# Optimization experiments

Measured on AMD Instinct MI355X. Metric: run time of the kernel, lower is better.

Reference implementation:

```python
import jax, jax.numpy as jnp
import numpy as np

D_MODEL = 1024
N_HEAD = 16
DFF = 4096
N_EXPERTS = 4
DFF_E = DFF // N_EXPERTS  # 1024, per-expert hidden
LN_EPS = 1e-5


def _layer_norm(x, g, b):
    m = jnp.mean(x, axis=-1, keepdims=True)
    v = jnp.mean(jnp.square(x - m), axis=-1, keepdims=True)
    return (x - m) * jax.lax.rsqrt(v + LN_EPS) * g + b


def setup_inputs() -> dict:
    key = jax.random.key(0)
    ks = jax.random.split(key, 16)
    B, S, D = 8, 1024, D_MODEL
    s = 0.02
    return {
        "src": jax.random.normal(ks[0], (B, S, D), jnp.float32),
        "pos_embed": jax.random.normal(ks[1], (B, S, D), jnp.float32),
        # nn.MultiheadAttention packed in-projection [3D, D] and out-projection [D, D]
        "in_proj_w": jax.random.normal(ks[2], (3 * D, D), jnp.float32) * s,
        "in_proj_b": jax.random.normal(ks[3], (3 * D,), jnp.float32) * s,
        "out_proj_w": jax.random.normal(ks[4], (D, D), jnp.float32) * s,
        "out_proj_b": jax.random.normal(ks[5], (D,), jnp.float32) * s,
        # MoE gate Linear(D, E)
        "gate_w": jax.random.normal(ks[6], (N_EXPERTS, D), jnp.float32) * s,
        "gate_b": jax.random.normal(ks[7], (N_EXPERTS,), jnp.float32) * s,
        # per-expert FFN: Linear(D, DFF_E) then Linear(DFF_E, D), stacked over experts
        "w1": jax.random.normal(ks[8], (N_EXPERTS, DFF_E, D), jnp.float32) * s,
        "b1": jax.random.normal(ks[9], (N_EXPERTS, DFF_E), jnp.float32) * s,
        "w2": jax.random.normal(ks[10], (N_EXPERTS, D, DFF_E), jnp.float32) * s,
        "b2": jax.random.normal(ks[11], (N_EXPERTS, D), jnp.float32) * s,
        # LayerNorms
        "ln1_g": jnp.ones((D,), jnp.float32),
        "ln1_b": jnp.zeros((D,), jnp.float32),
        "ln2_g": jnp.ones((D,), jnp.float32),
        "ln2_b": jnp.zeros((D,), jnp.float32),
    }


def reference(src, pos_embed, in_proj_w, in_proj_b, out_proj_w, out_proj_b,
              gate_w, gate_b, w1, b1, w2, b2, ln1_g, ln1_b, ln2_g, ln2_b):
    B, S, D = src.shape
    H, hd = N_HEAD, D // N_HEAD
    residual = src
    # --- self-attention (post-norm path, dropout in eval mode => identity) ---
    qk = src + pos_embed  # q = k = src + pos_embed, value = src
    wq, wk, wv = jnp.split(in_proj_w, 3, axis=0)
    bq, bk, bv = jnp.split(in_proj_b, 3)
    q = (qk @ wq.T + bq).reshape(B, S, H, hd).transpose(0, 2, 1, 3)
    k = (qk @ wk.T + bk).reshape(B, S, H, hd).transpose(0, 2, 1, 3)
    v = (src @ wv.T + bv).reshape(B, S, H, hd).transpose(0, 2, 1, 3)
    scores = jnp.einsum('bhqd,bhkd->bhqk', q, k) / jnp.sqrt(jnp.asarray(hd, q.dtype))
    attn = jax.nn.softmax(scores, axis=-1)
    o = jnp.einsum('bhqk,bhkd->bhqd', attn, v).transpose(0, 2, 1, 3).reshape(B, S, D)
    o = o @ out_proj_w.T + out_proj_b
    x = _layer_norm(residual + o, ln1_g, ln1_b)
    # --- MoE FFN: sample one expert per token from gate softmax ---
    gate_logits = x @ gate_w.T + gate_b  # [B, S, E]
    chosen = jax.random.categorical(jax.random.key(42), gate_logits, axis=-1)  # [B, S] int
    oh = jax.nn.one_hot(chosen, N_EXPERTS, dtype=x.dtype)  # [B, S, E]
    # dense all-expert compute + one-hot select (equals gather/scatter math)
    h = jax.nn.relu(jnp.einsum('bsd,efd->bsef', x, w1) + b1)  # [B,S,E,DFF_E]
    y = jnp.einsum('bsef,edf->bsed', h, w2) + b2              # [B,S,E,D]
    moe_out = jnp.einsum('bsed,bse->bsd', y, oh)
    out = _layer_norm(x + moe_out, ln2_g, ln2_b)
    return out
```

## Files before the change

kernel.cpp:

```cpp
#include <hip/hip_runtime.h>
#include <cstdint>
#include <cstddef>


typedef _Float16 h16;
typedef h16 h16x8 __attribute__((ext_vector_type(8)));
typedef h16 h16x4 __attribute__((ext_vector_type(4)));
typedef __fp16 fp16x2 __attribute__((ext_vector_type(2)));
typedef float f32x4 __attribute__((ext_vector_type(4)));
typedef uint32_t u32;

#define DM 1024
#define NH 16
#define HD 64
#define SEQ 1024
#define BB 8
#define BS (BB*SEQ)
#define NBH (BB*NH)
#define NE 4
#define DFE 1024
#define QB 128
#define NCHUNK 16
#define SLDA 32
#define FLD 72
#define NPOS 9216

#define MFMA16(a,b,c) __builtin_amdgcn_mfma_f32_16x16x32_f16(a,b,c,0,0,0)

static constexpr size_t E = (size_t)BS*DM*2;
static constexpr size_t OFF_QKH = 0;
static constexpr size_t OFF_QKL = E;
static constexpr size_t OFF_SRCH= 2*E;
static constexpr size_t OFF_SRCL= 3*E;
static constexpr size_t OFF_W3H = 4*E;
static constexpr size_t OFF_W3L = 4*E + (size_t)3*DM*DM*2;
static constexpr size_t OFF_WOH = 4*E + (size_t)6*DM*DM*2;
static constexpr size_t OFF_WOL = 4*E + (size_t)7*DM*DM*2;
static constexpr size_t OFF_QH  = 5*E;
static constexpr size_t OFF_QL  = 6*E;
static constexpr size_t OFF_KH  = 7*E;
static constexpr size_t OFF_KL  = 8*E;
static constexpr size_t OFF_VH  = 9*E;
static constexpr size_t OFF_VL  = 10*E;
static constexpr size_t OFF_OH  = 0;
static constexpr size_t OFF_OL  = E;
static constexpr size_t OFF_ATT = 2*E;
static constexpr size_t OFF_X   = 5*E;
static constexpr size_t OFF_XH  = 7*E;
static constexpr size_t OFF_W1H = 8*E;
static constexpr size_t OFF_W2H = 8*E + (size_t)NE*DFE*DM*2;
static constexpr size_t OFF_HH  = 9*E;
static constexpr size_t OFF_Y   = 11*E;
static constexpr size_t OFF_CHOSEN = 13*E;
static constexpr size_t OFF_COUNTS = 13*E + 32768;
static constexpr size_t OFF_CURSOR = OFF_COUNTS + 16;
static constexpr size_t OFF_EOFF   = OFF_CURSOR + 16;
static constexpr size_t OFF_PLIST  = OFF_EOFF + 16;
static constexpr size_t WS_NEEDED  = OFF_PLIST + (size_t)NPOS*4;

__device__ __forceinline__ void store_split(h16* H, h16* L, size_t idx, float v) {
  h16 h = (h16)v;
  H[idx] = h;
  L[idx] = (h16)(v - (float)h);
}

__device__ __forceinline__ float wave_sum(float v) {
  #pragma unroll
  for (int o = 32; o; o >>= 1) v += __shfl_xor(v, o);
  return v;
}

__device__ __forceinline__ u32 pk2(float a, float b, float& fa, float& fb) {
  union { fp16x2 h; u32 w; } u;
  u.h = __builtin_amdgcn_cvt_pkrtz(a, b);
  fa = (float)u.h[0];
  fb = (float)u.h[1];
  return u.w;
}
__device__ __forceinline__ u32 pk2w(float a, float b) {
  union { fp16x2 h; u32 w; } u;
  u.h = __builtin_amdgcn_cvt_pkrtz(a, b);
  return u.w;
}

__device__ __forceinline__ void gload16(const void* g, void* l) {
  __builtin_amdgcn_global_load_lds(
      (const __attribute__((address_space(1))) u32*)g,
      (__attribute__((address_space(3))) u32*)l, 16, 0, 0);
}

__device__ __forceinline__ void gemm256_core(
    const h16* __restrict__ Ah, const h16* __restrict__ Al,
    const h16* __restrict__ Bh, const h16* __restrict__ Bl,
    int K, int lda, int ldb, int m0, int n0,
    f32x4 (&acc)[8][4], h16* lds)
{
  constexpr int BUF = 4*256*SLDA;
  const int tid = threadIdx.x, lane = tid & 63, wid = tid >> 6;
  const int wr = (wid >> 2) * 128, wc = (wid & 3) * 64;
  const int lr16 = lane >> 2, lgrp = lane & 3;
  const int plane = wid >> 1;
  const int half  = (wid & 1) * 128;
  const int sw = (lr16 >> 1) & 3;
  const h16* gp = (plane == 0) ? Ah : (plane == 1) ? Al : (plane == 2) ? Bh : Bl;
  const int ld  = (plane < 2) ? lda : ldb;
  const long g0 = (long)((plane < 2 ? m0 : n0) + half + lr16) * ld + ((lgrp ^ sw) << 3);
  const int lo = plane*(256*SLDA) + half*SLDA;
  const int fr = lane & 15, gi = lane >> 4;
  const int pcol = ((gi ^ ((lane >> 1) & 3)) << 3);
  const int nt = K >> 5;

  auto stage = [&](int t, int buf) {
    h16* lbase = lds + buf*BUF + lo;
    const long k0 = (long)t << 5;
    #pragma unroll
    for (int g = 0; g < 8; ++g)
      gload16(gp + g0 + (long)(g*16)*ld + k0, lbase + (g*16)*SLDA);
  };

  stage(0, 0);
  __syncthreads();
  int cur = 0;
  for (int t = 0; t < nt; ++t) {
    if (t + 1 < nt) stage(t + 1, cur ^ 1);
    h16* base = lds + cur*BUF;
    h16* sAh_ = base;
    h16* sAl_ = base + 256*SLDA;
    h16* sBh_ = base + 2*256*SLDA;
    h16* sBl_ = base + 3*256*SLDA;
    h16x8 bh[4], bl[4];
    #pragma unroll
    for (int j = 0; j < 4; ++j) {
      bh[j] = *(const h16x8*)(sBh_ + (wc + j*16 + fr)*SLDA + pcol);
      bl[j] = *(const h16x8*)(sBl_ + (wc + j*16 + fr)*SLDA + pcol);
    }
    __builtin_amdgcn_s_setprio(1);
    #pragma unroll
    for (int i = 0; i < 8; ++i) {
      h16x8 ah = *(const h16x8*)(sAh_ + (wr + i*16 + fr)*SLDA + pcol);
      h16x8 al = *(const h16x8*)(sAl_ + (wr + i*16 + fr)*SLDA + pcol);
      #pragma unroll
      for (int j = 0; j < 4; ++j) {
        acc[i][j] = MFMA16(ah, bh[j], acc[i][j]);
        acc[i][j] = MFMA16(ah, bl[j], acc[i][j]);
        acc[i][j] = MFMA16(al, bh[j], acc[i][j]);
      }
    }
    __builtin_amdgcn_s_setprio(0);
    __syncthreads();
    cur ^= 1;
  }
}

#define EPI_256 \
  const int lane = threadIdx.x & 63, wid = threadIdx.x >> 6; \
  const int wr = (wid>>2)*128, wc = (wid&3)*64; \
  const int fr = lane & 15, rb = (lane>>4)*4;

template<bool GATHER>
__device__ __forceinline__ void hgemm256_core(
    const h16* __restrict__ A, const h16* __restrict__ B,
    int K, int lda, int ldb, int m0, int n0, const int* __restrict__ rowmap,
    f32x4 (&acc)[8][4], h16* lds)
{
  constexpr int BUF = 2*256*SLDA;
  const int tid = threadIdx.x, lane = tid & 63, wid = tid >> 6;
  const int wr = (wid >> 2) * 128, wc = (wid & 3) * 64;
  const int lr16 = lane >> 2, lgrp = lane & 3;
  const int plane = wid >> 2;
  const int qrow  = (wid & 3) * 64;
  const int sw = (lr16 >> 1) & 3;
  const int colo = (lgrp ^ sw) << 3;
  const h16* gp = plane ? B : A;
  const int ld  = plane ? ldb : lda;
  long g0[4];
  #pragma unroll
  for (int g = 0; g < 4; ++g) {
    int lrow = qrow + g*16 + lr16;
    long grow;
    if (GATHER && plane == 0) {
      int t = rowmap[m0 + lrow]; if (t < 0) t = 0;
      grow = t;
    } else {
      grow = (plane ? n0 : m0) + lrow;
    }
    g0[g] = grow * (long)ld + colo;
  }
  const int lo = plane*(256*SLDA) + qrow*SLDA;
  const int fr = lane & 15, gi = lane >> 4;
  const int pcol = ((gi ^ ((lane >> 1) & 3)) << 3);
  const int nt = K >> 5;

  auto stage = [&](int t, int buf) {
    h16* lbase = lds + buf*BUF + lo;
    const long k0 = (long)t << 5;
    #pragma unroll
    for (int g = 0; g < 4; ++g)
      gload16(gp + g0[g] + k0, lbase + (g*16)*SLDA);
  };

  stage(0, 0);
  __syncthreads();
  int cur = 0;
  for (int t = 0; t < nt; ++t) {
    if (t + 1 < nt) stage(t + 1, cur ^ 1);
    h16* base = lds + cur*BUF;
    h16* sA_ = base;
    h16* sB_ = base + 256*SLDA;
    h16x8 b_[4];
    #pragma unroll
    for (int j = 0; j < 4; ++j)
      b_[j] = *(const h16x8*)(sB_ + (wc + j*16 + fr)*SLDA + pcol);
    __builtin_amdgcn_s_setprio(1);
    #pragma unroll
    for (int i = 0; i < 8; ++i) {
      h16x8 a_ = *(const h16x8*)(sA_ + (wr + i*16 + fr)*SLDA + pcol);
      #pragma unroll
      for (int j = 0; j < 4; ++j)
        acc[i][j] = MFMA16(a_, b_[j], acc[i][j]);
    }
    __builtin_amdgcn_s_setprio(0);
    __syncthreads();
    cur ^= 1;
  }
}

__global__ void k_zero8(int* __restrict__ p) {
  if (threadIdx.x < 8) p[threadIdx.x] = 0;
}

__global__ void k_split_in(const float* __restrict__ src, const float* __restrict__ pos,
                           h16* __restrict__ qkH, h16* __restrict__ qkL,
                           h16* __restrict__ sH,  h16* __restrict__ sL) {
  int i = blockIdx.x*256 + threadIdx.x;
  float4 s = ((const float4*)src)[i];
  float4 p = ((const float4*)pos)[i];
  float sv[4] = {s.x, s.y, s.z, s.w};
  float qv[4] = {s.x+p.x, s.y+p.y, s.z+p.z, s.w+p.w};
  h16x4 sh, sl, qh, ql;
  #pragma unroll
  for (int q = 0; q < 4; ++q) {
    float xs = sv[q] * 16.0f; h16 hs = (h16)xs;
    sh[q] = hs; sl[q] = (h16)(xs - (float)hs);
    float xq = qv[q] * 16.0f; h16 hq = (h16)xq;
    qh[q] = hq; ql[q] = (h16)(xq - (float)hq);
  }
  ((h16x4*)sH)[i] = sh; ((h16x4*)sL)[i] = sl;
  ((h16x4*)qkH)[i] = qh; ((h16x4*)qkL)[i] = ql;
}

__global__ void k_split2(const float* __restrict__ a,
                         h16* __restrict__ H, h16* __restrict__ L, float scale, int n4) {
  int i = blockIdx.x*256 + threadIdx.x;
  if (i >= n4) return;
  float4 v = ((const float4*)a)[i];
  float vv[4] = {v.x, v.y, v.z, v.w};
  h16x4 hv, lv;
  #pragma unroll
  for (int q = 0; q < 4; ++q) {
    float x = vv[q] * scale;
    h16 h = (h16)x;
    hv[q] = h;
    lv[q] = (h16)(x - (float)h);
  }
  ((h16x4*)H)[i] = hv;
  ((h16x4*)L)[i] = lv;
}

__global__ void k_tof16(const float* __restrict__ a, h16* __restrict__ H, float scale, int n4) {
  int i = blockIdx.x*256 + threadIdx.x;
  if (i >= n4) return;
  float4 v = ((const float4*)a)[i];
  h16x4 hv;
  hv[0] = (h16)(v.x*scale); hv[1] = (h16)(v.y*scale);
  hv[2] = (h16)(v.z*scale); hv[3] = (h16)(v.w*scale);
  ((h16x4*)H)[i] = hv;
}

__global__ __launch_bounds__(512, 2) void k_qkv(
    const h16* __restrict__ qkh, const h16* __restrict__ qkl,
    const h16* __restrict__ sh,  const h16* __restrict__ sl,
    const h16* __restrict__ Wh,  const h16* __restrict__ Wl, const float* __restrict__ bias,
    h16* __restrict__ Qh, h16* __restrict__ Ql, h16* __restrict__ Kh, h16* __restrict__ Kl,
    h16* __restrict__ Vh, h16* __restrict__ Vl)
{
  __shared__ h16 lds[2*4*256*SLDA];
  const int bid = blockIdx.x;
  const int xcd = bid & 7, loc = bid >> 3;
  const int m0 = (xcd*4 + (loc & 3)) * 256;
  const int n0 = (loc >> 2) * 256;
  const bool isV = (n0 >= 2048);
  f32x4 acc[8][4] = {};
  gemm256_core(isV ? sh : qkh, isV ? sl : qkl, Wh, Wl,
               1024, 1024, 1024, m0, n0, acc, lds);
  EPI_256;
  if (!isV) {
    const bool isK = (n0 >= 1024);
    h16* Hd = isK ? Kh : Qh;
    h16* Ld = isK ? Kl : Ql;
    #pragma unroll
    for (int i = 0; i < 8; ++i)
      #pragma unroll
      for (int j = 0; j < 4; ++j)
        #pragma unroll
        for (int r = 0; r < 4; ++r) {
          int row = m0 + wr + i*16 + rb + r;
          int col = n0 + wc + j*16 + fr;
          float c = acc[i][j][r] * (1.0f/1024.0f) + bias[col];
          int b = row >> 10, s = row & 1023;
          int cc = col & 1023, h = cc >> 6, d = cc & 63;
          long bh = (long)b*NH + h;
          store_split(Hd, Ld, (bh*SEQ + s)*HD + d, c * 16.0f);
        }
  } else {
    #pragma unroll
    for (int i = 0; i < 8; ++i)
      #pragma unroll
      for (int j = 0; j < 4; ++j) {
        int row0 = m0 + wr + i*16 + rb;
        int col  = n0 + wc + j*16 + fr;
        int cc = col & 1023, h = cc >> 6, d = cc & 63;
        float bcol = bias[col];
        h16x4 hv, lv;
        #pragma unroll
        for (int r = 0; r < 4; ++r) {
          float cs = (acc[i][j][r] * (1.0f/1024.0f) + bcol) * 16.0f;
          h16 hh = (h16)cs;
          hv[r] = hh;
          lv[r] = (h16)(cs - (float)hh);
        }
        int b = row0 >> 10, s0 = row0 & 1023;
        long base = ((long)(b*NH + h)*HD + d)*SEQ + s0;
        *(h16x4*)(Vh + base) = hv;
        *(h16x4*)(Vl + base) = lv;
      }
  }
}

__global__ __launch_bounds__(512) void k_attn(
    const h16* __restrict__ Qh, const h16* __restrict__ Ql,
    const h16* __restrict__ Kh, const h16* __restrict__ Kl,
    const h16* __restrict__ Vh, const h16* __restrict__ Vl,
    h16* __restrict__ Oh, h16* __restrict__ Ol)
{
  __shared__ h16 lds[4*64*FLD];
  h16* sKh = lds;            h16* sKl = lds + 64*FLD;
  h16* sVh = lds + 2*64*FLD; h16* sVl = lds + 3*64*FLD;
  const int bid = blockIdx.x;
  const int swz = (bid & 7) * 128 + (bid >> 3);
  const int bh = swz >> 3;
  const int q0 = (swz & 7) * QB;
  const int tid = threadIdx.x, lane = tid & 63, w = tid >> 6;
  const int fr = lane & 15, hg = lane >> 4;
  const int kg = hg << 3;
  const long qbase = ((long)bh*SEQ + q0 + w*16 + fr) * HD;
  h16x8 qh[2], ql[2];
  qh[0] = *(const h16x8*)(Qh + qbase + kg);
  qh[1] = *(const h16x8*)(Qh + qbase + 32 + kg);
  ql[0] = *(const h16x8*)(Ql + qbase + kg);
  ql[1] = *(const h16x8*)(Ql + qbase + 32 + kg);
  f32x4 o1[4] = {}, o2[4] = {};
  float mrow = -3.0e38f, lrow = 0.f;
  const int srow = tid >> 3, skc = (tid & 7) << 3;
  const long kbase = ((long)bh*SEQ + srow) * HD + skc;
  const long vbase = ((long)bh*HD + srow) * SEQ + skc;
  const int srcA = fr + ((hg & 1) << 5);
  const int srcB = srcA + 16;
  uint4 rKh, rKl, rVh, rVl;
  auto loadt = [&](int kt) {
    const long ka = kbase + (long)(kt*64)*HD;
    rKh = *(const uint4*)(Kh + ka);
    rKl = *(const uint4*)(Kl + ka);
    const long va = vbase + kt*64;
    rVh = *(const uint4*)(Vh + va);
    rVl = *(const uint4*)(Vl + va);
  };
  loadt(0);
  for (int kt = 0; kt < NCHUNK; ++kt) {
    __syncthreads();
    *(uint4*)(sKh + srow*FLD + skc) = rKh;
    *(uint4*)(sKl + srow*FLD + skc) = rKl;
    *(uint4*)(sVh + srow*FLD + skc) = rVh;
    *(uint4*)(sVl + srow*FLD + skc) = rVl;
    __syncthreads();
    if (kt + 1 < NCHUNK) loadt(kt + 1);
    f32x4 s1[4] = {}, s2[4] = {};
    __builtin_amdgcn_s_setprio(1);
    #pragma unroll
    for (int ks = 0; ks < 2; ++ks)
      #pragma unroll
      for (int j = 0; j < 4; ++j) {
        h16x8 kh = *(const h16x8*)(sKh + (j*16 + fr)*FLD + ks*32 + kg);
        h16x8 kl = *(const h16x8*)(sKl + (j*16 + fr)*FLD + ks*32 + kg);
        s1[j] = MFMA16(kh, qh[ks], s1[j]);
        s2[j] = MFMA16(kh, ql[ks], s2[j]);
        s2[j] = MFMA16(kl, qh[ks], s2[j]);
      }
    __builtin_amdgcn_s_setprio(0);
    float p[4][4];
    float tmax = -3.0e38f;
    #pragma unroll
    for (int j = 0; j < 4; ++j)
      #pragma unroll
      for (int r = 0; r < 4; ++r) {
        float sc = (s1[j][r] + s2[j][r]) * (0.125f/256.0f);
        p[j][r] = sc;
        tmax = fmaxf(tmax, sc);
      }
    tmax = fmaxf(tmax, __shfl_xor(tmax, 16));
    tmax = fmaxf(tmax, __shfl_xor(tmax, 32));
    float mn;
    const bool defer = (__all(tmax - mrow <= 4.0f) != 0);
    float sclf;
    if (defer) {
      mn = mrow;
      sclf = 1.0f;
    } else {
      mn = fmaxf(mrow, tmax);
      sclf = __expf(mrow - mn);
      mrow = mn;
    }
    float psum = 0.f;
    #pragma unroll
    for (int j = 0; j < 4; ++j)
      #pragma unroll
      for (int r = 0; r < 4; ++r) { float e = __expf(p[j][r] - mn); p[j][r] = e; psum += e; }
    psum += __shfl_xor(psum, 16);
    psum += __shfl_xor(psum, 32);
    lrow = lrow*sclf + psum;
    if (!defer) {
      #pragma unroll
      for (int r = 0; r < 4; ++r) {
        float sq = __shfl(sclf, hg*4 + r);
        #pragma unroll
        for (int jd = 0; jd < 4; ++jd) { o1[jd][r] *= sq; o2[jd][r] *= sq; }
      }
    }
    u32 hp[4][2], lp[4][2];
    #pragma unroll
    for (int j = 0; j < 4; ++j)
      #pragma unroll
      for (int rp = 0; rp < 2; ++rp) {
        float a = p[j][2*rp]   * 512.0f;
        float b = p[j][2*rp+1] * 512.0f;
        float fa, fb;
        hp[j][rp] = pk2(a, b, fa, fb);
        lp[j][rp] = pk2w(a - fa, b - fb);
      }
    #pragma unroll
    for (int ks = 0; ks < 2; ++ks) {
      const int j0 = 2*ks, j1 = 2*ks + 1;
      u32 hA0 = (u32)__shfl((int)hp[j0][0], srcA), hA1 = (u32)__shfl((int)hp[j0][1], srcA);
      u32 hB0 = (u32)__shfl((int)hp[j0][0], srcB), hB1 = (u32)__shfl((int)hp[j0][1], srcB);
      u32 hC0 = (u32)__shfl((int)hp[j1][0], srcA), hC1 = (u32)__shfl((int)hp[j1][1], srcA);
      u32 hD0 = (u32)__shfl((int)hp[j1][0], srcB), hD1 = (u32)__shfl((int)hp[j1][1], srcB);
      u32 lA0 = (u32)__shfl((int)lp[j0][0], srcA), lA1 = (u32)__shfl((int)lp[j0][1], srcA);
      u32 lB0 = (u32)__shfl((int)lp[j0][0], srcB), lB1 = (u32)__shfl((int)lp[j0][1], srcB);
      u32 lC0 = (u32)__shfl((int)lp[j1][0], srcA), lC1 = (u32)__shfl((int)lp[j1][1], srcA);
      u32 lD0 = (u32)__shfl((int)lp[j1][0], srcB), lD1 = (u32)__shfl((int)lp[j1][1], srcB);
      const bool hij = (hg & 2) != 0;
      union { u32 w[4]; h16x8 v; } pa, pb;
      pa.w[0] = hij ? hC0 : hA0;  pa.w[1] = hij ? hC1 : hA1;
      pa.w[2] = hij ? hD0 : hB0;  pa.w[3] = hij ? hD1 : hB1;
      pb.w[0] = hij ? lC0 : lA0;  pb.w[1] = hij ? lC1 : lA1;
      pb.w[2] = hij ? lD0 : lB0;  pb.w[3] = hij ? lD1 : lB1;
      __builtin_amdgcn_s_setprio(1);
      #pragma unroll
      for (int jd = 0; jd < 4; ++jd) {
        h16x8 vh = *(const h16x8*)(sVh + (jd*16 + fr)*FLD + ks*32 + kg);
        h16x8 vl = *(const h16x8*)(sVl + (jd*16 + fr)*FLD + ks*32 + kg);
        o1[jd] = MFMA16(pa.v, vh, o1[jd]);
        o2[jd] = MFMA16(pa.v, vl, o2[jd]);
        o2[jd] = MFMA16(pb.v, vh, o2[jd]);
      }
      __builtin_amdgcn_s_setprio(0);
    }
  }
  float lq[4];
  #pragma unroll
  for (int r = 0; r < 4; ++r) lq[r] = __shfl(lrow, hg*4 + r);
  const int b = bh >> 4, h = bh & 15;
  #pragma unroll
  for (int jd = 0; jd < 4; ++jd)
    #pragma unroll
    for (int r = 0; r < 4; ++r) {
      int qrow = q0 + w*16 + hg*4 + r;
      int d = jd*16 + fr;
      float ov = (o1[jd][r] + o2[jd][r]) / (512.0f*16.0f*lq[r]);
      store_split(Oh, Ol, ((long)b*SEQ + qrow)*DM + h*HD + d, ov*16.0f);
    }
}

__global__ __launch_bounds__(512, 2) void k_out(
    const h16* __restrict__ Oh, const h16* __restrict__ Ol,
    const h16* __restrict__ Wh, const h16* __restrict__ Wl,
    const float* __restrict__ bias, float* __restrict__ attn)
{
  __shared__ h16 lds[2*4*256*SLDA];
  const int bid = blockIdx.x;
  const int xcd = bid & 7, loc = bid >> 3;
  const int m0 = (xcd*4 + (loc & 3)) * 256;
  const int n0 = (loc >> 2) * 256;
  f32x4 acc[8][4] = {};
  gemm256_core(Oh, Ol, Wh, Wl, 1024, 1024, 1024, m0, n0, acc, lds);
  EPI_256;
  #pragma unroll
  for (int i = 0; i < 8; ++i)
    #pragma unroll
    for (int j = 0; j < 4; ++j)
      #pragma unroll
      for (int r = 0; r < 4; ++r) {
        int row = m0 + wr + i*16 + rb + r;
        int col = n0 + wc + j*16 + fr;
        attn[(long)row*DM + col] = acc[i][j][r] * (1.0f/1024.0f) + bias[col];
      }
}

__device__ __forceinline__ void threefry(u32 x0, u32 x1, u32& y0, u32& y1) {
  const u32 ks0 = 0u, ks1 = 42u, ks2 = 0x1BD11BDAu ^ 42u;
  x0 += ks0; x1 += ks1;
  #define TF_R(r) { x0 += x1; x1 = (x1 << r) | (x1 >> (32 - r)); x1 ^= x0; }
  TF_R(13) TF_R(15) TF_R(26) TF_R(6)  x0 += ks1; x1 += ks2 + 1u;
  TF_R(17) TF_R(29) TF_R(16) TF_R(24) x0 += ks2; x1 += ks0 + 2u;
  TF_R(13) TF_R(15) TF_R(26) TF_R(6)  x0 += ks0; x1 += ks1 + 3u;
  TF_R(17) TF_R(29) TF_R(16) TF_R(24) x0 += ks1; x1 += ks2 + 4u;
  TF_R(13) TF_R(15) TF_R(26) TF_R(6)  x0 += ks2; x1 += ks0 + 5u;
  #undef TF_R
  y0 = x0; y1 = x1;
}

__device__ __forceinline__ float gumbel_from(u32 bits) {
  float f = __uint_as_float((bits >> 9) | 0x3F800000u) - 1.0f;
  float u = (f > 0.0f) ? f : 1.17549435e-38f;
  float nl = (float)(-log((double)u));
  return -(float)log((double)nl);
}

__global__ __launch_bounds__(256) void k_ln1g(
    const float* __restrict__ A, const float* __restrict__ Badd,
    const float* __restrict__ g, const float* __restrict__ be,
    const float* __restrict__ gw, const float* __restrict__ gb,
    float* __restrict__ xout, h16* __restrict__ xh,
    int* __restrict__ chosen, int* __restrict__ counts)
{
  int wave = threadIdx.x >> 6, lane = threadIdx.x & 63;
  long row = (long)blockIdx.x*4 + wave;
  const float* ar = A + row*DM; const float* br = Badd + row*DM;
  float v[16]; float s = 0.0f;
  #pragma unroll
  for (int p = 0; p < 4; ++p) {
    int d = p*256 + lane*4;
    float4 a = *(const float4*)(ar + d);
    float4 b = *(const float4*)(br + d);
    float t0=a.x+b.x, t1=a.y+b.y, t2=a.z+b.z, t3=a.w+b.w;
    v[4*p+0]=t0; v[4*p+1]=t1; v[4*p+2]=t2; v[4*p+3]=t3;
    s += t0+t1+t2+t3;
  }
  s = wave_sum(s);
  float m = s * (1.0f/1024.0f);
  float q = 0.0f;
  #pragma unroll
  for (int i = 0; i < 16; ++i) { float dd = v[i]-m; q += dd*dd; }
  q = wave_sum(q);
  float rs = (float)(1.0 / sqrt((double)(q * (1.0f/1024.0f) + 1e-5f)));
  float pe[4] = {0.f, 0.f, 0.f, 0.f};
  #pragma unroll
  for (int p = 0; p < 4; ++p) {
    int d = p*256 + lane*4;
    float4 gv = *(const float4*)(g + d);
    float4 bv = *(const float4*)(be + d);
    float y0 = (v[4*p+0]-m)*rs*gv.x + bv.x;
    float y1 = (v[4*p+1]-m)*rs*gv.y + bv.y;
    float y2 = (v[4*p+2]-m)*rs*gv.z + bv.z;
    float y3 = (v[4*p+3]-m)*rs*gv.w + bv.w;
    float4 o = {y0,y1,y2,y3};
    *(float4*)(xout + row*DM + d) = o;
    h16x4 hv; hv[0]=(h16)(y0*16.f); hv[1]=(h16)(y1*16.f);
    hv[2]=(h16)(y2*16.f); hv[3]=(h16)(y3*16.f);
    *(h16x4*)(xh + row*DM + d) = hv;
    #pragma unroll
    for (int e = 0; e < 4; ++e) {
      float4 w4 = *(const float4*)(gw + e*DM + d);
      pe[e] += y0*w4.x + y1*w4.y + y2*w4.z + y3*w4.w;
    }
  }
  #pragma unroll
  for (int e = 0; e < 4; ++e) pe[e] = wave_sum(pe[e]);
  if (lane == 0) {
    float best = -3.0e38f; int arg = 0;
    #pragma unroll
    for (int e = 0; e < 4; ++e) {
      float logit = pe[e] + gb[e];
      u32 j = (u32)(4*row + e);
      u32 y0, y1;
      threefry(0u, j, y0, y1);
      float vv = gumbel_from(y0 ^ y1) + logit;
      if (vv > best) { best = vv; arg = e; }
    }
    chosen[(int)row] = arg;
    atomicAdd(&counts[arg], 1);
  }
}

__global__ __launch_bounds__(256) void k_ln(
    const float* __restrict__ A, const float* __restrict__ Badd,
    const float* __restrict__ g, const float* __restrict__ be,
    float* __restrict__ dout)
{
  int wave = threadIdx.x >> 6, lane = threadIdx.x & 63;
  long row = (long)blockIdx.x*4 + wave;
  const float* ar = A + row*DM; const float* br = Badd + row*DM;
  float v[16]; float s = 0.0f;
  #pragma unroll
  for (int p = 0; p < 4; ++p) {
    int d = p*256 + lane*4;
    float4 a = *(const float4*)(ar + d);
    float4 b = *(const float4*)(br + d);
    float t0=a.x+b.x, t1=a.y+b.y, t2=a.z+b.z, t3=a.w+b.w;
    v[4*p+0]=t0; v[4*p+1]=t1; v[4*p+2]=t2; v[4*p+3]=t3;
    s += t0+t1+t2+t3;
  }
  s = wave_sum(s);
  float m = s * (1.0f/1024.0f);
  float q = 0.0f;
  #pragma unroll
  for (int i = 0; i < 16; ++i) { float dd = v[i]-m; q += dd*dd; }
  q = wave_sum(q);
  float rs = (float)(1.0 / sqrt((double)(q * (1.0f/1024.0f) + 1e-5f)));
  #pragma unroll
  for (int p = 0; p < 4; ++p) {
    int d = p*256 + lane*4;
    float4 gv = *(const float4*)(g + d);
    float4 bv = *(const float4*)(be + d);
    float y0 = (v[4*p+0]-m)*rs*gv.x + bv.x;
    float y1 = (v[4*p+1]-m)*rs*gv.y + bv.y;
    float y2 = (v[4*p+2]-m)*rs*gv.z + bv.z;
    float y3 = (v[4*p+3]-m)*rs*gv.w + bv.w;
    float4 o = {y0,y1,y2,y3};
    *(float4*)(dout + row*DM + d) = o;
  }
}

__global__ void k_offsets(const int* __restrict__ counts, int* __restrict__ eoff) {
  if (threadIdx.x == 0 && blockIdx.x == 0) {
    int o = 0;
    for (int e = 0; e < 4; ++e) { eoff[e] = o; o += (counts[e] + 255) & ~255; }
  }
}

__global__ void k_fill(int* __restrict__ p, int n) {
  int i = blockIdx.x*256 + threadIdx.x;
  if (i < n) p[i] = -1;
}

__global__ void k_scatter(const int* __restrict__ chosen, const int* __restrict__ eoff,
                          int* __restrict__ cursor, int* __restrict__ plist) {
  int t = blockIdx.x*256 + threadIdx.x;
  if (t >= BS) return;
  int e = chosen[t];
  int slot = atomicAdd(&cursor[e], 1);
  plist[eoff[e] + slot] = t;
}

__global__ __launch_bounds__(512, 2) void k_e1(
    const h16* __restrict__ Xh, const h16* __restrict__ W1, const float* __restrict__ b1,
    const int* __restrict__ plist, const int* __restrict__ eoff, h16* __restrict__ Hh)
{
  __shared__ h16 lds[2*2*256*SLDA];
  const int n0 = blockIdx.x*256, m0 = blockIdx.y*256;
  const int e = (m0 >= eoff[1]) + (m0 >= eoff[2]) + (m0 >= eoff[3]);
  f32x4 acc[8][4] = {};
  hgemm256_core<true>(Xh, W1 + (long)e*DFE*DM, 1024, 1024, 1024, m0, n0, plist, acc, lds);
  EPI_256;
  #pragma unroll
  for (int i = 0; i < 8; ++i)
    #pragma unroll
    for (int j = 0; j < 4; ++j)
      #pragma unroll
      for (int r = 0; r < 4; ++r) {
        int row = m0 + wr + i*16 + rb + r;
        int col = n0 + wc + j*16 + fr;
        float c = acc[i][j][r] * (1.0f/1024.0f) + b1[e*DFE + col];
        c = fmaxf(c, 0.0f);
        Hh[(long)row*DFE + col] = (h16)(c * 16.0f);
      }
}

__global__ __launch_bounds__(512, 2) void k_e2(
    const h16* __restrict__ Hh, const h16* __restrict__ W2, const float* __restrict__ b2,
    const int* __restrict__ plist, const int* __restrict__ eoff, float* __restrict__ y)
{
  __shared__ h16 lds[2*2*256*SLDA];
  const int n0 = blockIdx.x*256, m0 = blockIdx.y*256;
  const int e = (m0 >= eoff[1]) + (m0 >= eoff[2]) + (m0 >= eoff[3]);
  f32x4 acc[8][4] = {};
  hgemm256_core<false>(Hh, W2 + (long)e*DM*DFE, 1024, DFE, DFE, m0, n0, nullptr, acc, lds);
  EPI_256;
  #pragma unroll
  for (int i = 0; i < 8; ++i)
    #pragma unroll
    for (int j = 0; j < 4; ++j)
      #pragma unroll
      for (int r = 0; r < 4; ++r) {
        int row = m0 + wr + i*16 + rb + r;
        int col = n0 + wc + j*16 + fr;
        int t = plist[row];
        if (t >= 0)
          y[(long)t*DM + col] = acc[i][j][r] * (1.0f/1024.0f) + b2[e*DM + col];
      }
}

extern "C" void kernel_launch(void* const* d_in, const int* in_sizes, int n_in,
                              void* d_out, int out_size, void* d_ws, size_t ws_size,
                              hipStream_t stream) {
  const float* src = (const float*)d_in[0];
  const float* pos = (const float*)d_in[1];
  const float* w3  = (const float*)d_in[2];
  const float* b3  = (const float*)d_in[3];
  const float* wo  = (const float*)d_in[4];
  const float* bo  = (const float*)d_in[5];
  const float* gw  = (const float*)d_in[6];
  const float* gb  = (const float*)d_in[7];
  const float* w1  = (const float*)d_in[8];
  const float* b1  = (const float*)d_in[9];
  const float* w2  = (const float*)d_in[10];
  const float* b2  = (const float*)d_in[11];
  const float* g1  = (const float*)d_in[12];
  const float* be1 = (const float*)d_in[13];
  const float* g2  = (const float*)d_in[14];
  const float* be2 = (const float*)d_in[15];
  float* out = (float*)d_out;
  char* ws = (char*)d_ws;
  if (ws_size < WS_NEEDED) return;

  auto H = [&](size_t off) { return (h16*)(ws + off); };
  auto F = [&](size_t off) { return (float*)(ws + off); };
  auto I = [&](size_t off) { return (int*)(ws + off); };

  k_zero8<<<1, 64, 0, stream>>>(I(OFF_COUNTS));

  k_split_in<<<BS*DM/4/256, 256, 0, stream>>>(src, pos,
      H(OFF_QKH), H(OFF_QKL), H(OFF_SRCH), H(OFF_SRCL));
  k_split2<<<3*DM*DM/4/256, 256, 0, stream>>>(w3, H(OFF_W3H), H(OFF_W3L), 64.0f, 3*DM*DM/4);
  k_split2<<<DM*DM/4/256, 256, 0, stream>>>(wo, H(OFF_WOH), H(OFF_WOL), 64.0f, DM*DM/4);

  k_qkv<<<dim3(384), 512, 0, stream>>>(
      H(OFF_QKH), H(OFF_QKL), H(OFF_SRCH), H(OFF_SRCL), H(OFF_W3H), H(OFF_W3L), b3,
      H(OFF_QH), H(OFF_QL), H(OFF_KH), H(OFF_KL), H(OFF_VH), H(OFF_VL));

  k_attn<<<dim3(NBH*(SEQ/QB)), 512, 0, stream>>>(
      H(OFF_QH), H(OFF_QL), H(OFF_KH), H(OFF_KL), H(OFF_VH), H(OFF_VL),
      H(OFF_OH), H(OFF_OL));

  k_out<<<dim3(128), 512, 0, stream>>>(
      H(OFF_OH), H(OFF_OL), H(OFF_WOH), H(OFF_WOL), bo, F(OFF_ATT));
  k_ln1g<<<BS/4, 256, 0, stream>>>(src, F(OFF_ATT), g1, be1, gw, gb,
      F(OFF_X), H(OFF_XH), I(OFF_CHOSEN), I(OFF_COUNTS));

  k_offsets<<<1, 64, 0, stream>>>(I(OFF_COUNTS), I(OFF_EOFF));
  k_fill<<<(NPOS+255)/256, 256, 0, stream>>>(I(OFF_PLIST), NPOS);
  k_scatter<<<BS/256, 256, 0, stream>>>(I(OFF_CHOSEN), I(OFF_EOFF), I(OFF_CURSOR), I(OFF_PLIST));

  k_tof16<<<NE*DFE*DM/4/256, 256, 0, stream>>>(w1, H(OFF_W1H), 64.0f, NE*DFE*DM/4);
  k_tof16<<<NE*DM*DFE/4/256, 256, 0, stream>>>(w2, H(OFF_W2H), 64.0f, NE*DM*DFE/4);
  k_e1<<<dim3(DFE/256, NPOS/256), 512, 0, stream>>>(
      H(OFF_XH), H(OFF_W1H), b1, I(OFF_PLIST), I(OFF_EOFF), H(OFF_HH));
  k_e2<<<dim3(DM/256, NPOS/256), 512, 0, stream>>>(
      H(OFF_HH), H(OFF_W2H), b2, I(OFF_PLIST), I(OFF_EOFF), F(OFF_Y));

  k_ln<<<BS/4, 256, 0, stream>>>(F(OFF_X), F(OFF_Y), g2, be2, out);
}
```

Measured before the change: 690.6 us.

## Shrink split-fp16 QKV and out-projection GEMM tiles to 128x256

Replaces the 256x256 three-MFMA split-precision GEMM core with a 128x256 tile, so k_qkv launches 768 blocks and k_out 256 blocks instead of 384 and 128. The staging loader is rewritten to spread 768 LDS rows over 8 waves, 6 loads each. This gives better CU coverage on a 256-CU part, especially for k_out, which previously had only 128 blocks. The cost is lower per-block arithmetic intensity and more redundant B-tile loads. The launch bounds hint drops the min-2-blocks requirement.

```diff
diff --git a/kernel.cpp b/kernel.cpp
--- a/kernel.cpp
+++ b/kernel.cpp
@@ -89,33 +89,44 @@
       (__attribute__((address_space(3))) u32*)l, 16, 0, 0);
 }
 
-__device__ __forceinline__ void gemm256_core(
+__device__ __forceinline__ void gemm128x256_core(
     const h16* __restrict__ Ah, const h16* __restrict__ Al,
     const h16* __restrict__ Bh, const h16* __restrict__ Bl,
     int K, int lda, int ldb, int m0, int n0,
-    f32x4 (&acc)[8][4], h16* lds)
-{
-  constexpr int BUF = 4*256*SLDA;
+    f32x4 (&acc)[4][4], h16* lds)
+{
+  constexpr int ROWS = 768;
+  constexpr int BUF = ROWS*SLDA;
   const int tid = threadIdx.x, lane = tid & 63, wid = tid >> 6;
-  const int wr = (wid >> 2) * 128, wc = (wid & 3) * 64;
+  const int wr = (wid >> 2) * 64, wc = (wid & 3) * 64;
   const int lr16 = lane >> 2, lgrp = lane & 3;
-  const int plane = wid >> 1;
-  const int half  = (wid & 1) * 128;
   const int sw = (lr16 >> 1) & 3;
-  const h16* gp = (plane == 0) ? Ah : (plane == 1) ? Al : (plane == 2) ? Bh : Bl;
-  const int ld  = (plane < 2) ? lda : ldb;
-  const long g0 = (long)((plane < 2 ? m0 : n0) + half + lr16) * ld + ((lgrp ^ sw) << 3);
-  const int lo = plane*(256*SLDA) + half*SLDA;
+  const int colo = (lgrp ^ sw) << 3;
+  const h16* gptr[6];
+  long gaddr[6];
+  int ldsoff[6];
+  #pragma unroll
+  for (int g = 0; g < 6; ++g) {
+    const int R0 = wid*96 + g*16;
+    const h16* gp; int prow, ld, base0;
+    if (R0 < 128)      { gp = Ah; prow = R0;       ld = lda; base0 = m0; }
+    else if (R0 < 256) { gp = Al; prow = R0 - 128; ld = lda; base0 = m0; }
+    else if (R0 < 512) { gp = Bh; prow = R0 - 256; ld = ldb; base0 = n0; }
+    else               { gp = Bl; prow = R0 - 512; ld = ldb; base0 = n0; }
+    gptr[g]   = gp;
+    gaddr[g]  = (long)(base0 + prow + lr16) * ld + colo;
+    ldsoff[g] = R0 * SLDA;
+  }
   const int fr = lane & 15, gi = lane >> 4;
   const int pcol = ((gi ^ ((lane >> 1) & 3)) << 3);
   const int nt = K >> 5;
 
   auto stage = [&](int t, int buf) {
-    h16* lbase = lds + buf*BUF + lo;
     const long k0 = (long)t << 5;
-    #pragma unroll
-    for (int g = 0; g < 8; ++g)
-      gload16(gp + g0 + (long)(g*16)*ld + k0, lbase + (g*16)*SLDA);
+    h16* lbase = lds + buf*BUF;
+    #pragma unroll
+    for (int g = 0; g < 6; ++g)
+      gload16(gptr[g] + gaddr[g] + k0, lbase + ldsoff[g]);
   };
 
   stage(0, 0);
@@ -125,9 +136,9 @@
     if (t + 1 < nt) stage(t + 1, cur ^ 1);
     h16* base = lds + cur*BUF;
     h16* sAh_ = base;
-    h16* sAl_ = base + 256*SLDA;
-    h16* sBh_ = base + 2*256*SLDA;
-    h16* sBl_ = base + 3*256*SLDA;
+    h16* sAl_ = base + 128*SLDA;
+    h16* sBh_ = base + 256*SLDA;
+    h16* sBl_ = base + 512*SLDA;
     h16x8 bh[4], bl[4];
     #pragma unroll
     for (int j = 0; j < 4; ++j) {
@@ -136,7 +147,7 @@
     }
     __builtin_amdgcn_s_setprio(1);
     #pragma unroll
-    for (int i = 0; i < 8; ++i) {
+    for (int i = 0; i < 4; ++i) {
       h16x8 ah = *(const h16x8*)(sAh_ + (wr + i*16 + fr)*SLDA + pcol);
       h16x8 al = *(const h16x8*)(sAl_ + (wr + i*16 + fr)*SLDA + pcol);
       #pragma unroll
@@ -151,6 +162,11 @@
     cur ^= 1;
   }
 }
+
+#define EPI_128x256 \
+  const int lane = threadIdx.x & 63, wid = threadIdx.x >> 6; \
+  const int wr = (wid>>2)*64, wc = (wid&3)*64; \
+  const int fr = lane & 15, rb = (lane>>4)*4;
 
 #define EPI_256 \
   const int lane = threadIdx.x & 63, wid = threadIdx.x >> 6; \
@@ -277,29 +293,29 @@
   ((h16x4*)H)[i] = hv;
 }
 
-__global__ __launch_bounds__(512, 2) void k_qkv(
+__global__ __launch_bounds__(512) void k_qkv(
     const h16* __restrict__ qkh, const h16* __restrict__ qkl,
     const h16* __restrict__ sh,  const h16* __restrict__ sl,
     const h16* __restrict__ Wh,  const h16* __restrict__ Wl, const float* __restrict__ bias,
     h16* __restrict__ Qh, h16* __restrict__ Ql, h16* __restrict__ Kh, h16* __restrict__ Kl,
     h16* __restrict__ Vh, h16* __restrict__ Vl)
 {
-  __shared__ h16 lds[2*4*256*SLDA];
+  __shared__ h16 lds[2*768*SLDA];
   const int bid = blockIdx.x;
   const int xcd = bid & 7, loc = bid >> 3;
-  const int m0 = (xcd*4 + (loc & 3)) * 256;
-  const int n0 = (loc >> 2) * 256;
+  const int m0 = (xcd*8 + (loc & 7)) * 128;
+  const int n0 = (loc >> 3) * 256;
   const bool isV = (n0 >= 2048);
-  f32x4 acc[8][4] = {};
-  gemm256_core(isV ? sh : qkh, isV ? sl : qkl, Wh, Wl,
-               1024, 1024, 1024, m0, n0, acc, lds);
-  EPI_256;
+  f32x4 acc[4][4] = {};
+  gemm128x256_core(isV ? sh : qkh, isV ? sl : qkl, Wh, Wl,
+                   1024, 1024, 1024, m0, n0, acc, lds);
+  EPI_128x256;
   if (!isV) {
     const bool isK = (n0 >= 1024);
     h16* Hd = isK ? Kh : Qh;
     h16* Ld = isK ? Kl : Ql;
     #pragma unroll
-    for (int i = 0; i < 8; ++i)
+    for (int i = 0; i < 4; ++i)
       #pragma unroll
       for (int j = 0; j < 4; ++j)
         #pragma unroll
@@ -314,7 +330,7 @@
         }
   } else {
     #pragma unroll
-    for (int i = 0; i < 8; ++i)
+    for (int i = 0; i < 4; ++i)
       #pragma unroll
       for (int j = 0; j < 4; ++j) {
         int row0 = m0 + wr + i*16 + rb;
@@ -491,21 +507,21 @@
     }
 }
 
-__global__ __launch_bounds__(512, 2) void k_out(
+__global__ __launch_bounds__(512) void k_out(
     const h16* __restrict__ Oh, const h16* __restrict__ Ol,
     const h16* __restrict__ Wh, const h16* __restrict__ Wl,
     const float* __restrict__ bias, float* __restrict__ attn)
 {
-  __shared__ h16 lds[2*4*256*SLDA];
+  __shared__ h16 lds[2*768*SLDA];
   const int bid = blockIdx.x;
   const int xcd = bid & 7, loc = bid >> 3;
-  const int m0 = (xcd*4 + (loc & 3)) * 256;
-  const int n0 = (loc >> 2) * 256;
-  f32x4 acc[8][4] = {};
-  gemm256_core(Oh, Ol, Wh, Wl, 1024, 1024, 1024, m0, n0, acc, lds);
-  EPI_256;
-  #pragma unroll
-  for (int i = 0; i < 8; ++i)
+  const int m0 = (xcd*8 + (loc & 7)) * 128;
+  const int n0 = (loc >> 3) * 256;
+  f32x4 acc[4][4] = {};
+  gemm128x256_core(Oh, Ol, Wh, Wl, 1024, 1024, 1024, m0, n0, acc, lds);
+  EPI_128x256;
+  #pragma unroll
+  for (int i = 0; i < 4; ++i)
     #pragma unroll
     for (int j = 0; j < 4; ++j)
       #pragma unroll
@@ -744,7 +760,7 @@
   k_split2<<<3*DM*DM/4/256, 256, 0, stream>>>(w3, H(OFF_W3H), H(OFF_W3L), 64.0f, 3*DM*DM/4);
   k_split2<<<DM*DM/4/256, 256, 0, stream>>>(wo, H(OFF_WOH), H(OFF_WOL), 64.0f, DM*DM/4);
 
-  k_qkv<<<dim3(384), 512, 0, stream>>>(
+  k_qkv<<<dim3(768), 512, 0, stream>>>(
       H(OFF_QKH), H(OFF_QKL), H(OFF_SRCH), H(OFF_SRCL), H(OFF_W3H), H(OFF_W3L), b3,
       H(OFF_QH), H(OFF_QL), H(OFF_KH), H(OFF_KL), H(OFF_VH), H(OFF_VL));
 
@@ -752,7 +768,7 @@
       H(OFF_QH), H(OFF_QL), H(OFF_KH), H(OFF_KL), H(OFF_VH), H(OFF_VL),
       H(OFF_OH), H(OFF_OL));
 
-  k_out<<<dim3(128), 512, 0, stream>>>(
+  k_out<<<dim3(256), 512, 0, stream>>>(
       H(OFF_OH), H(OFF_OL), H(OFF_WOH), H(OFF_WOL), bo, F(OFF_ATT));
   k_ln1g<<<BS/4, 256, 0, stream>>>(src, F(OFF_ATT), g1, be1, gw, gb,
       F(OFF_X), H(OFF_XH), I(OFF_CHOSEN), I(OFF_COUNTS));
```

Measured after the change: 672.8 us. -2.6%, faster.
